# Optimization experiments

Measured on AMD Instinct MI355X. Metric: run time of the kernel, lower is better.

Reference implementation:

```python
import jax, jax.numpy as jnp
import numpy as np

B, IN, U = 16, 1024, 1024


def _wSw(W, S):
    # W: [i,u], S: [b,i,i] -> W^T S W : [b,u,u]
    return jnp.einsum('iu,bij,jv->buv', W, S, W)


def _xSx(x, Wsig):
    # (sum_i x_i^2) * W_Sigma, broadcast over batch
    return jnp.sum(x * x, axis=1)[:, None, None] * Wsig


def _trS(S, Wsig):
    return jnp.trace(S, axis1=1, axis2=2)[:, None, None] * Wsig


def _hadamard_sigma(s1, s2, m1, m2):
    # s1*s2 + diag(m1) s2 diag(m1) + diag(m2) s1 diag(m2)
    return (s1 * s2
            + m1[:, :, None] * s2 * m1[:, None, :]
            + m2[:, :, None] * s1 * m2[:, None, :])


def _act_sigma(g, S):
    # S * outer(g, g)
    return S * (g[:, :, None] * g[:, None, :])


def setup_inputs() -> dict:
    key = jax.random.key(0)
    ks = jax.random.split(key, 16)
    f32 = jnp.float32
    init_mu, ini_sigma = 0.05, -4.6
    inp = {
        'mu_inputs': jax.random.normal(ks[0], (B, IN), f32),
        'sigma_inputs': 0.01 * jax.random.normal(ks[1], (B, IN, IN), f32),
        'prev_state': 0.1 * jax.random.normal(ks[2], (B, U), f32),
        'Sigma_state': 0.01 * jax.random.normal(ks[3], (B, U, U), f32),
        'U_z': init_mu * jax.random.normal(ks[4], (IN, U), f32),
        'uz_sigma': jnp.full((U,), ini_sigma, f32),
        'W_z': init_mu * jax.random.normal(ks[5], (U, U), f32),
        'wz_sigma': jnp.full((U,), ini_sigma, f32),
        'U_r': init_mu * jax.random.normal(ks[6], (IN, U), f32),
        'ur_sigma': jnp.full((U,), ini_sigma, f32),
        'W_r': init_mu * jax.random.normal(ks[7], (U, U), f32),
        'wr_sigma': jnp.full((U,), ini_sigma, f32),
        'U_h': init_mu * jax.random.normal(ks[8], (IN, U), f32),
        'uh_sigma': jnp.full((U,), ini_sigma, f32),
        'W_h': init_mu * jax.random.normal(ks[9], (U, U), f32),
        'wh_sigma': jnp.full((U,), ini_sigma, f32),
    }
    return inp


def reference(mu_inputs, sigma_inputs, prev_state, Sigma_state,
              U_z, uz_sigma, W_z, wz_sigma,
              U_r, ur_sigma, W_r, wr_sigma,
              U_h, uh_sigma, W_h, wh_sigma):
    sp = jax.nn.softplus
    # ---- z gate ----
    pre_z = mu_inputs @ U_z + prev_state @ W_z
    z = jax.nn.sigmoid(pre_z)
    Uz_S, Wz_S = jnp.diag(sp(uz_sigma)), jnp.diag(sp(wz_sigma))
    Sigma_zz = (_wSw(U_z, sigma_inputs) + _xSx(mu_inputs, Uz_S) + _trS(sigma_inputs, Uz_S)
                + _wSw(W_z, Sigma_state) + _xSx(prev_state, Wz_S) + _trS(Sigma_state, Wz_S))
    Sigma_z = _act_sigma(z * (1.0 - z), Sigma_zz)  # analytic d sigmoid
    # ---- r gate ----
    pre_r = mu_inputs @ U_r + prev_state @ W_r
    r = jax.nn.sigmoid(pre_r)
    Ur_S, Wr_S = jnp.diag(sp(ur_sigma)), jnp.diag(sp(wr_sigma))
    Sigma_rr = (_wSw(U_r, sigma_inputs) + _xSx(mu_inputs, Ur_S) + _trS(sigma_inputs, Ur_S)
                + _wSw(W_r, Sigma_state) + _xSx(prev_state, Wr_S) + _trS(Sigma_state, Wr_S))
    Sigma_r = _act_sigma(r * (1.0 - r), Sigma_rr)
    # ---- h gate ----
    sr = prev_state * r
    pre_h = mu_inputs @ U_h + sr @ W_h
    h = jnp.tanh(pre_h)
    Uh_S, Wh_S = jnp.diag(sp(uh_sigma)), jnp.diag(sp(wh_sigma))
    sigma_g = _hadamard_sigma(Sigma_state, Sigma_r, prev_state, r)
    Sigma_hh = (_wSw(U_h, sigma_inputs) + _xSx(mu_inputs, Uh_S) + _trS(sigma_inputs, Uh_S)
                + _wSw(W_h, sigma_g) + _xSx(sr, Wh_S) + _trS(sigma_g, Wh_S))
    Sigma_h = _act_sigma(1.0 - h * h, Sigma_hh)  # analytic d tanh
    # ---- combine ----
    mu_out = z * prev_state + (1.0 - z) * h
    sigma_a = _hadamard_sigma(Sigma_z, Sigma_state, z, prev_state)
    sigma_b = _hadamard_sigma(Sigma_z, Sigma_h, 1.0 - z, h)
    sigma_ab = Sigma_z * (prev_state[:, :, None] * h[:, None, :])
    sigma_abT = Sigma_z * (h[:, :, None] * prev_state[:, None, :])
    Sigma_out = sigma_a + sigma_b - sigma_ab - sigma_abT
    Sigma_out = jnp.where(jnp.isfinite(Sigma_out), Sigma_out, jnp.zeros_like(Sigma_out))
    eye = jnp.eye(Sigma_out.shape[-1], dtype=bool)
    Sigma_out = jnp.where(eye, jnp.abs(Sigma_out), Sigma_out)
    return mu_out, Sigma_out
```

## Files before the change

kernel.cpp:

```cpp
#include <hip/hip_runtime.h>
#include <math.h>


#define B_  16
#define N_  1024
#define NN_ (1024*1024)

typedef __bf16 bf16x8 __attribute__((ext_vector_type(8)));
typedef float  f32x4  __attribute__((ext_vector_type(4)));
typedef unsigned short ushort8v __attribute__((ext_vector_type(8)));

__device__ __forceinline__ unsigned short f2bf(float f) {
  union { float f; unsigned int u; } v; v.f = f;
  unsigned int r = v.u + 0x7fffu + ((v.u >> 16) & 1u);
  return (unsigned short)(r >> 16);
}
__device__ __forceinline__ float bf2f(unsigned short h) {
  union { unsigned int u; float f; } v; v.u = ((unsigned int)h) << 16;
  return v.f;
}
__device__ __forceinline__ float f4get(const float4& v, int q) {
  return q == 0 ? v.x : (q == 1 ? v.y : (q == 2 ? v.z : v.w));
}
__device__ __forceinline__ unsigned short u4get(const ushort4& v, int q) {
  return q == 0 ? v.x : (q == 1 ? v.y : (q == 2 ? v.z : v.w));
}

__device__ __forceinline__ void gload_lds16(const void* g, void* l) {
  __builtin_amdgcn_global_load_lds((__attribute__((address_space(1))) void*)g,
                                   (__attribute__((address_space(3))) void*)l,
                                   16, 0, 0);
}

#define MFMA_ __builtin_amdgcn_mfma_f32_16x16x32_bf16

template<int OMODE, int PAIR>
__global__ __launch_bounds__(512)
void gemm8p(const unsigned short* __restrict__ A, int lda, long aStride, int koffA,
            const unsigned short* __restrict__ Bm, const unsigned short* __restrict__ Bm2,
            int ldb, long bStride, int K,
            void* __restrict__ Out, int ldo, long oStride, int noff,
            const float* __restrict__ act,
            const float* __restrict__ spU, const float* __restrict__ spW,
            const float* __restrict__ dU, const float* __restrict__ dW)
{
  __shared__ __align__(16) char ldsb[131072];
  const int id = blockIdx.x;
  const int xcd = id & 7, rest = id >> 3;
  const int mt = rest & 3, pp = rest >> 2;
  const int panel = xcd + (pp << 3);
  const int nt = panel & 3;
  const int b  = (panel >> 2) & 15;
  const int ps = PAIR ? (panel >> 6) : 0;
  const unsigned short* Bsel = (PAIR && ps) ? Bm2 : Bm;
  const int kofx = koffA + (ps ? 1024 : 0);
  const int nofx = noff  + (ps ? 1024 : 0);
  const int mbase = mt << 8, nbase = nt << 8;
  const int tid = threadIdx.x, lane = tid & 63, w = tid >> 6;
  const int wm = w >> 2, wn = w & 3;
  const int NT = K >> 6;

  f32x4 acc[8][4];
  const f32x4 zero4 = {0.f, 0.f, 0.f, 0.f};
#pragma unroll
  for (int i = 0; i < 8; i++)
#pragma unroll
    for (int j = 0; j < 4; j++) acc[i][j] = zero4;

  const int l3 = lane >> 3, l7 = lane & 7;
  const int posg = l7 ^ l3;
  const int gr = (l3 << 1) + (posg >> 2);
  const int gc = (posg & 3) << 3;
  const int bi0 = w << 1, bi1 = bi0 + 1;
  const int rS0 = ((bi0 >> 1) << 4) + gr, cS0 = ((bi0 & 1) << 5) + gc;
  const int rS1 = ((bi1 >> 1) << 4) + gr, cS1 = ((bi1 & 1) << 5) + gc;
  const unsigned short* Ab = A + (size_t)b * aStride + (size_t)mbase * lda + kofx;
  const unsigned short* Bb = Bsel + (size_t)b * bStride + (size_t)nbase * ldb;
  const int d0 = w << 11, d1 = (w << 11) + 1024;

  auto SA = [&](int tt, int h) {
    char* dst = ldsb + ((tt & 1) << 16) + (h << 14);
    const unsigned short* s = Ab + (size_t)(h << 7) * lda + ((size_t)tt << 6);
    gload_lds16(s + (size_t)rS0 * lda + cS0, dst + d0);
    gload_lds16(s + (size_t)rS1 * lda + cS1, dst + d1);
  };
  auto SB = [&](int tt, int h) {
    char* dst = ldsb + ((tt & 1) << 16) + 32768 + (h << 14);
    const unsigned short* s = Bb + (size_t)(h << 7) * ldb + ((size_t)tt << 6);
    gload_lds16(s + (size_t)rS0 * ldb + cS0, dst + d0);
    gload_lds16(s + (size_t)rS1 * ldb + cS1, dst + d1);
  };

  const int lrow = lane & 15, c4 = lane >> 4;
  const int aoff = ((lrow >> 1) << 7) + (((((lrow & 1) << 2) | c4) ^ (lrow >> 1)) << 4);
  const int abase = wm << 14;
  const int bbase = 32768 + ((wn >> 1) << 14);
  const int brg   = (wn & 1) << 2;
  auto LDA = [&](const char* pb, int mi, int ks) -> bf16x8 {
    return *(const bf16x8*)(pb + abase + (((mi << 1) + ks) << 10) + aoff);
  };
  auto LDB = [&](const char* pb, int ni, int ks) -> bf16x8 {
    return *(const bf16x8*)(pb + bbase + ((((brg + ni) << 1) + ks) << 10) + aoff);
  };

  SA(0, 0); SA(0, 1); SB(0, 0); SB(0, 1);
  if (NT > 1) { SB(1, 0); SA(1, 0); }
  asm volatile("s_waitcnt vmcnt(4)" ::: "memory");
  __builtin_amdgcn_sched_barrier(0);
  __builtin_amdgcn_s_barrier();
  __builtin_amdgcn_sched_barrier(0);

  bf16x8 av[4][2], bv[4][2];
  for (int kt = 0; kt < NT; ++kt) {
    const char* pb = ldsb + ((kt & 1) << 16);
#pragma unroll
    for (int mi = 0; mi < 4; mi++)
#pragma unroll
      for (int ks = 0; ks < 2; ks++) av[mi][ks] = LDA(pb, mi, ks);
#pragma unroll
    for (int ni = 0; ni < 2; ni++)
#pragma unroll
      for (int ks = 0; ks < 2; ks++) bv[ni][ks] = LDB(pb, ni, ks);
    if (kt + 1 < NT) SB(kt + 1, 1);
    __builtin_amdgcn_s_barrier();
    asm volatile("s_waitcnt lgkmcnt(0)" ::: "memory");
    __builtin_amdgcn_sched_barrier(0);
    __builtin_amdgcn_s_setprio(1);
#pragma unroll
    for (int ni = 0; ni < 2; ni++)
#pragma unroll
      for (int mi = 0; mi < 4; mi++) {
        acc[mi][ni] = MFMA_(av[mi][0], bv[ni][0], acc[mi][ni], 0, 0, 0);
        acc[mi][ni] = MFMA_(av[mi][1], bv[ni][1], acc[mi][ni], 0, 0, 0);
      }
    __builtin_amdgcn_s_setprio(0);
    __builtin_amdgcn_sched_barrier(0);
    __builtin_amdgcn_s_barrier();
#pragma unroll
    for (int ni = 2; ni < 4; ni++)
#pragma unroll
      for (int ks = 0; ks < 2; ks++) bv[ni][ks] = LDB(pb, ni, ks);
    if (kt + 1 < NT) SA(kt + 1, 1);
    __builtin_amdgcn_s_barrier();
    asm volatile("s_waitcnt lgkmcnt(0)" ::: "memory");
    __builtin_amdgcn_sched_barrier(0);
    __builtin_amdgcn_s_setprio(1);
#pragma unroll
    for (int ni = 2; ni < 4; ni++)
#pragma unroll
      for (int mi = 0; mi < 4; mi++) {
        acc[mi][ni] = MFMA_(av[mi][0], bv[ni][0], acc[mi][ni], 0, 0, 0);
        acc[mi][ni] = MFMA_(av[mi][1], bv[ni][1], acc[mi][ni], 0, 0, 0);
      }
    __builtin_amdgcn_s_setprio(0);
    __builtin_amdgcn_sched_barrier(0);
    __builtin_amdgcn_s_barrier();
#pragma unroll
    for (int mi = 0; mi < 4; mi++)
#pragma unroll
      for (int ks = 0; ks < 2; ks++) av[mi][ks] = LDA(pb, 4 + mi, ks);
    if (kt + 2 < NT) SB(kt + 2, 0);
    __builtin_amdgcn_s_barrier();
    asm volatile("s_waitcnt lgkmcnt(0)" ::: "memory");
    __builtin_amdgcn_sched_barrier(0);
    __builtin_amdgcn_s_setprio(1);
#pragma unroll
    for (int ni = 0; ni < 2; ni++)
#pragma unroll
      for (int mi = 0; mi < 4; mi++) {
        acc[4 + mi][ni] = MFMA_(av[mi][0], bv[ni][0], acc[4 + mi][ni], 0, 0, 0);
        acc[4 + mi][ni] = MFMA_(av[mi][1], bv[ni][1], acc[4 + mi][ni], 0, 0, 0);
      }
    __builtin_amdgcn_s_setprio(0);
    __builtin_amdgcn_sched_barrier(0);
    __builtin_amdgcn_s_barrier();
    if (kt + 2 < NT) {
      SA(kt + 2, 0);
      asm volatile("s_waitcnt vmcnt(4)" ::: "memory");
    } else {
      asm volatile("s_waitcnt vmcnt(0)" ::: "memory");
    }
    __builtin_amdgcn_sched_barrier(0);
    __builtin_amdgcn_s_barrier();
    __builtin_amdgcn_sched_barrier(0);
    __builtin_amdgcn_s_setprio(1);
#pragma unroll
    for (int ni = 2; ni < 4; ni++)
#pragma unroll
      for (int mi = 0; mi < 4; mi++) {
        acc[4 + mi][ni] = MFMA_(av[mi][0], bv[ni][0], acc[4 + mi][ni], 0, 0, 0);
        acc[4 + mi][ni] = MFMA_(av[mi][1], bv[ni][1], acc[4 + mi][ni], 0, 0, 0);
      }
    __builtin_amdgcn_s_setprio(0);
    __builtin_amdgcn_sched_barrier(0);
    __builtin_amdgcn_s_barrier();
  }

  if (OMODE == 2) {
    const float* actb = act + b * N_;
    const float dUb = dU[b], dWb = dW[b];
#pragma unroll
    for (int mi = 0; mi < 8; mi++) {
      const int u0 = mbase + wm * 128 + mi * 16 + ((lane >> 4) << 2);
#pragma unroll
      for (int ni = 0; ni < 4; ni++) {
        const int v = nbase + wn * 64 + ni * 16 + (lane & 15);
        const float avv = actb[v];
#pragma unroll
        for (int r = 0; r < 4; r++) {
          const int u = u0 + r;
          float val = acc[mi][ni][r];
          if (u == v) val += dUb * spU[u] + dWb * spW[u];
          val *= actb[u] * avv;
          ((float*)Out)[(size_t)b * oStride + (size_t)u * ldo + v] = val;
        }
      }
    }
  } else {
    __syncthreads();
    unsigned short* scr = (unsigned short*)(ldsb + w * 16384);
    const float* actb = (OMODE == 1) ? (act + b * N_) : nullptr;
    float dUb = 0.f, dWb = 0.f;
    if (OMODE == 1) { dUb = dU[b]; dWb = dW[b]; }
#pragma unroll
    for (int mi = 0; mi < 8; mi++) {
      const int rl0 = mi * 16 + ((lane >> 4) << 2);
#pragma unroll
      for (int ni = 0; ni < 4; ni++) {
        const int cl = ni * 16 + (lane & 15);
#pragma unroll
        for (int r = 0; r < 4; r++) {
          const int rl = rl0 + r;
          float val = acc[mi][ni][r];
          if (OMODE == 1) {
            const int u = mbase + wm * 128 + rl, v = nbase + wn * 64 + cl;
            if (u == v) val += dUb * spU[u] + dWb * spW[u];
            val *= actb[u] * actb[v];
          }
          scr[rl * 64 + ((((cl >> 3) ^ (rl & 7))) << 3) + (cl & 7)] = f2bf(val);
        }
      }
    }
    asm volatile("s_waitcnt lgkmcnt(0)" ::: "memory");
    __builtin_amdgcn_sched_barrier(0);
    unsigned short* ob = (unsigned short*)Out + (size_t)b * oStride
        + (size_t)(mbase + wm * 128) * ldo + nofx + nbase + wn * 64;
#pragma unroll
    for (int pq = 0; pq < 16; pq++) {
      const int row = pq * 8 + (lane >> 3);
      const int ch = (lane & 7) ^ (row & 7);
      ushort8v vv = *(const ushort8v*)&scr[row * 64 + ((lane & 7) << 3)];
      *(ushort8v*)(ob + (size_t)row * ldo + ch * 8) = vv;
    }
  }
}


__global__ void conv_bf16(const float* __restrict__ in, unsigned short* __restrict__ out, int n4)
{
  int i = blockIdx.x * 256 + threadIdx.x;
  const int stride = gridDim.x * 256;
  for (; i < n4; i += stride) {
    const float4 v = ((const float4*)in)[i];
    ushort4 o;
    o.x = f2bf(v.x); o.y = f2bf(v.y); o.z = f2bf(v.z); o.w = f2bf(v.w);
    ((ushort4*)out)[i] = o;
  }
}

__global__ void build_AT(const float* __restrict__ Uz, const float* __restrict__ Wz,
                         const float* __restrict__ Ur, const float* __restrict__ Wr,
                         const float* __restrict__ Uh, const float* __restrict__ Wh,
                         unsigned short* __restrict__ AT)
{
  __shared__ float tile[32][33];
  const int g = blockIdx.z;
  const float* U = g == 0 ? Uz : (g == 1 ? Ur : Uh);
  const float* W = g == 0 ? Wz : (g == 1 ? Wr : Wh);
  const int u0  = blockIdx.x * 32;
  const int k0g = blockIdx.y * 32;
  const float* src = (k0g >= 1024) ? W : U;
  const int kloc = k0g & 1023;
  const int tx = threadIdx.x & 31, ty = threadIdx.x >> 5;
  unsigned short* out = AT + (size_t)g * N_ * 2048;
#pragma unroll
  for (int i = 0; i < 32; i += 8) tile[ty + i][tx] = src[(size_t)(kloc + ty + i) * N_ + u0 + tx];
  __syncthreads();
#pragma unroll
  for (int i = 0; i < 32; i += 8)
    out[(size_t)(u0 + ty + i) * 2048 + k0g + tx] = f2bf(tile[tx][ty + i]);
}

__global__ void softplus6(const float* a0, const float* a1, const float* a2,
                          const float* a3, const float* a4, const float* a5,
                          float* __restrict__ sp)
{
  const float* src[6] = {a0, a1, a2, a3, a4, a5};
  const int g = blockIdx.x;
  const float* s = src[g];
  for (int i = threadIdx.x; i < N_; i += 256) {
    float x = s[i];
    sp[g * N_ + i] = (x > 20.f) ? x : log1pf(expf(x));
  }
}

__global__ void scalars1(const float* __restrict__ mu, const float* __restrict__ prev,
                         const float* __restrict__ sin_, const float* __restrict__ Sst,
                         float* __restrict__ dA, float* __restrict__ dBzr)
{
  __shared__ float red[256];
  const int b = blockIdx.x;
  float s1 = 0.f, s2 = 0.f;
  for (int i = threadIdx.x; i < N_; i += 256) {
    const float m = mu[b * N_ + i];
    s1 += m * m + sin_[(size_t)b * NN_ + (size_t)i * (N_ + 1)];
    const float p = prev[b * N_ + i];
    s2 += p * p + Sst[(size_t)b * NN_ + (size_t)i * (N_ + 1)];
  }
  red[threadIdx.x] = s1; __syncthreads();
  for (int s = 128; s > 0; s >>= 1) { if (threadIdx.x < s) red[threadIdx.x] += red[threadIdx.x + s]; __syncthreads(); }
  if (threadIdx.x == 0) dA[b] = red[0];
  __syncthreads();
  red[threadIdx.x] = s2; __syncthreads();
  for (int s = 128; s > 0; s >>= 1) { if (threadIdx.x < s) red[threadIdx.x] += red[threadIdx.x + s]; __syncthreads(); }
  if (threadIdx.x == 0) dBzr[b] = red[0];
}

__global__ __launch_bounds__(256)
void gate_pre2(const float* __restrict__ x1, const float* __restrict__ x2,
               const float* __restrict__ U0, const float* __restrict__ W0,
               const float* __restrict__ U1, const float* __restrict__ W1,
               float* __restrict__ Ppart)
{
  const int g  = blockIdx.z;
  const int ks = blockIdx.y;
  const int out = blockIdx.x * 256 + threadIdx.x;
  const int b = out >> 10, col = out & 1023;
  const float* x = (ks < 4) ? x1 : x2;
  const float* Wm = (g == 0) ? ((ks < 4) ? U0 : W0) : ((ks < 4) ? U1 : W1);
  const int k0 = (ks & 3) * 256;
  const float* xb = x + b * N_ + k0;
  const float* wp = Wm + (size_t)k0 * N_ + col;
  float acc = 0.f;
#pragma unroll 8
  for (int k = 0; k < 256; k++)
    acc += xb[k] * wp[(size_t)k * N_];
  Ppart[(g * 8 + ks) * (B_ * N_) + out] = acc;
}

__global__ void gate_act2(const float* __restrict__ P,
                          float* __restrict__ z, float* __restrict__ gz,
                          float* __restrict__ r, float* __restrict__ gr)
{
  const int out = blockIdx.x * 256 + threadIdx.x;
  float a0 = 0.f, a1 = 0.f;
#pragma unroll
  for (int ks = 0; ks < 8; ks++) {
    a0 += P[ks * (B_ * N_) + out];
    a1 += P[(8 + ks) * (B_ * N_) + out];
  }
  const float s0 = 1.f / (1.f + expf(-a0));
  const float s1 = 1.f / (1.f + expf(-a1));
  z[out] = s0; gz[out] = s0 * (1.f - s0);
  r[out] = s1; gr[out] = s1 * (1.f - s1);
}

__global__ __launch_bounds__(256)
void gate_pre1(const float* __restrict__ x1, const float* __restrict__ x2,
               const float* __restrict__ U0, const float* __restrict__ W0,
               float* __restrict__ Ppart)
{
  const int ks = blockIdx.y;
  const int out = blockIdx.x * 256 + threadIdx.x;
  const int b = out >> 10, col = out & 1023;
  const float* x = (ks < 4) ? x1 : x2;
  const float* Wm = (ks < 4) ? U0 : W0;
  const int k0 = (ks & 3) * 256;
  const float* xb = x + b * N_ + k0;
  const float* wp = Wm + (size_t)k0 * N_ + col;
  float acc = 0.f;
#pragma unroll 8
  for (int k = 0; k < 256; k++)
    acc += xb[k] * wp[(size_t)k * N_];
  Ppart[ks * (B_ * N_) + out] = acc;
}

__global__ void gate_act1(const float* __restrict__ P,
                          float* __restrict__ h, float* __restrict__ gh)
{
  const int out = blockIdx.x * 256 + threadIdx.x;
  float a0 = 0.f;
#pragma unroll
  for (int ks = 0; ks < 8; ks++) a0 += P[ks * (B_ * N_) + out];
  const float s = tanhf(a0);
  h[out] = s; gh[out] = 1.f - s * s;
}

__global__ void sr_csr(const float* __restrict__ prev, const float* __restrict__ r,
                       float* __restrict__ sr, float* __restrict__ csr)
{
  __shared__ float red[256];
  const int b = blockIdx.x;
  float s = 0.f;
  for (int i = threadIdx.x; i < N_; i += 256) {
    const float v = prev[b * N_ + i] * r[b * N_ + i];
    sr[b * N_ + i] = v;
    s += v * v;
  }
  red[threadIdx.x] = s; __syncthreads();
  for (int k = 128; k > 0; k >>= 1) { if (threadIdx.x < k) red[threadIdx.x] += red[threadIdx.x + k]; __syncthreads(); }
  if (threadIdx.x == 0) csr[b] = red[0];
}

__global__ void hadamard_sg(const float* __restrict__ Sst, unsigned short* __restrict__ Sg,
                            const float* __restrict__ prev, const float* __restrict__ r)
{
  const size_t idx = ((size_t)blockIdx.x * 256 + threadIdx.x) * 4;
  const int b = (int)(idx >> 20);
  const int rem = (int)(idx & (NN_ - 1));
  const int i = rem >> 10, j0 = rem & 1023;
  const float pi = prev[b * N_ + i], ri = r[b * N_ + i];
  const float4  ss  = *(const float4*)(Sst + (size_t)b * NN_ + rem);
  const ushort4 sr4 = *(const ushort4*)(Sg + (size_t)b * NN_ + rem);
  ushort4 o;
  unsigned short* op = (unsigned short*)&o;
#pragma unroll
  for (int q = 0; q < 4; q++) {
    const float srv = bf2f(u4get(sr4, q));
    const float stv = f4get(ss, q);
    const float pj = prev[b * N_ + j0 + q];
    const float rj = r[b * N_ + j0 + q];
    op[q] = f2bf(stv * srv + pi * pj * srv + ri * rj * stv);
  }
  *(ushort4*)(Sg + (size_t)b * NN_ + rem) = o;
}

__global__ void scalars2(const unsigned short* __restrict__ Sg,
                         const float* __restrict__ csr, float* __restrict__ dBh)
{
  __shared__ float red[256];
  const int b = blockIdx.x;
  float s = 0.f;
  for (int i = threadIdx.x; i < N_; i += 256)
    s += bf2f(Sg[(size_t)b * NN_ + (size_t)i * (N_ + 1)]);
  red[threadIdx.x] = s; __syncthreads();
  for (int k = 128; k > 0; k >>= 1) { if (threadIdx.x < k) red[threadIdx.x] += red[threadIdx.x + k]; __syncthreads(); }
  if (threadIdx.x == 0) dBh[b] = red[0] + csr[b];
}

__global__ void mu_kernel(const float* __restrict__ z, const float* __restrict__ prev,
                          const float* __restrict__ h, float* __restrict__ mu_out)
{
  const int i = blockIdx.x * 256 + threadIdx.x;
  const float zz = z[i];
  mu_out[i] = zz * prev[i] + (1.f - zz) * h[i];
}

__global__ void combine(const unsigned short* __restrict__ Sz, const float* __restrict__ Sst,
                        const float* __restrict__ z, const float* __restrict__ prev,
                        const float* __restrict__ h, float* __restrict__ SigOut)
{
  const int row = blockIdx.x;
  const int b = row >> 10, u = row & 1023;
  const float zu = z[b * N_ + u], pu = prev[b * N_ + u], hu = h[b * N_ + u];
  const size_t base = (size_t)b * NN_ + (size_t)u * N_;
  const int j0 = threadIdx.x * 4;
  const ushort4 s4 = *(const ushort4*)(Sz + base + j0);
  const float4 sh = *(const float4*)(SigOut + base + j0);
  const float4 st = *(const float4*)(Sst + base + j0);
  const float4 zv = *(const float4*)(z + b * N_ + j0);
  const float4 pv = *(const float4*)(prev + b * N_ + j0);
  const float4 hv = *(const float4*)(h + b * N_ + j0);
  float o[4];
#pragma unroll
  for (int q = 0; q < 4; q++) {
    const int v = j0 + q;
    const float sz  = bf2f(u4get(s4, q));
    const float shh = f4get(sh, q);
    const float stt = f4get(st, q);
    const float zvv = f4get(zv, q);
    const float pvv = f4get(pv, q);
    const float hvv = f4get(hv, q);
    float res = sz * stt + zu * zvv * stt + pu * pvv * sz
              + sz * shh + (1.f - zu) * (1.f - zvv) * shh + hu * hvv * sz
              - sz * (pu * hvv) - sz * (hu * pvv);
    if (!isfinite(res)) res = 0.f;
    if (u == v) res = fabsf(res);
    o[q] = res;
  }
  float4 ov; ov.x = o[0]; ov.y = o[1]; ov.z = o[2]; ov.w = o[3];
  *(float4*)(SigOut + base + j0) = ov;
}


extern "C" void kernel_launch(void* const* d_in, const int* in_sizes, int n_in,
                              void* d_out, int out_size, void* d_ws, size_t ws_size,
                              hipStream_t stream)
{
  const float* mu   = (const float*)d_in[0];
  const float* sin_ = (const float*)d_in[1];
  const float* prev = (const float*)d_in[2];
  const float* Sst  = (const float*)d_in[3];
  const float* Uz = (const float*)d_in[4];  const float* uzs = (const float*)d_in[5];
  const float* Wz = (const float*)d_in[6];  const float* wzs = (const float*)d_in[7];
  const float* Ur = (const float*)d_in[8];  const float* urs = (const float*)d_in[9];
  const float* Wr = (const float*)d_in[10]; const float* wrs = (const float*)d_in[11];
  const float* Uh = (const float*)d_in[12]; const float* uhs = (const float*)d_in[13];
  const float* Wh = (const float*)d_in[14]; const float* whs = (const float*)d_in[15];

  char* ws = (char*)d_ws;
  size_t off = 0;
  auto take = [&](size_t bytes) -> char* {
    char* p = ws + off;
    off = (off + bytes + 255) & ~(size_t)255;
    return p;
  };
  unsigned short* Tcm = (unsigned short*)take((size_t)B_ * 2048 * 1024 * 2);
  unsigned short* Sz  = (unsigned short*)take((size_t)B_ * NN_ * 2);
  unsigned short* Sg  = (unsigned short*)take((size_t)B_ * NN_ * 2);
  unsigned short* AT  = (unsigned short*)take((size_t)3 * N_ * 2048 * 2);
  float* Ppart = (float*)take((size_t)16 * B_ * N_ * 4);
  float* sp   = (float*)take(6 * N_ * 4);
  float* z    = (float*)take(B_ * N_ * 4);
  float* gz   = (float*)take(B_ * N_ * 4);
  float* rr   = (float*)take(B_ * N_ * 4);
  float* gr   = (float*)take(B_ * N_ * 4);
  float* h    = (float*)take(B_ * N_ * 4);
  float* gh   = (float*)take(B_ * N_ * 4);
  float* sr   = (float*)take(B_ * N_ * 4);
  float* dA   = (float*)take(64);
  float* dBzr = (float*)take(64);
  float* dBh  = (float*)take(64);
  float* csr  = (float*)take(64);
  if (off > ws_size) return;

  float* mu_out = (float*)d_out;
  float* SigOut = (float*)d_out + (size_t)B_ * N_;
  unsigned short* SinH = (unsigned short*)SigOut;
  unsigned short* SstH = (unsigned short*)SigOut + (size_t)B_ * NN_;

  const unsigned short* ATz = AT;
  const unsigned short* ATr = AT + (size_t)N_ * 2048;
  const unsigned short* ATh = AT + (size_t)2 * N_ * 2048;

  conv_bf16<<<2048, 256, 0, stream>>>(sin_, SinH, B_ * NN_ / 4);
  conv_bf16<<<2048, 256, 0, stream>>>(Sst,  SstH, B_ * NN_ / 4);
  softplus6<<<6, 256, 0, stream>>>(uzs, wzs, urs, wrs, uhs, whs, sp);
  scalars1<<<16, 256, 0, stream>>>(mu, prev, sin_, Sst, dA, dBzr);
  build_AT<<<dim3(32, 64, 3), 256, 0, stream>>>(Uz, Wz, Ur, Wr, Uh, Wh, AT);
  gate_pre2<<<dim3(64, 8, 2), 256, 0, stream>>>(mu, prev, Uz, Wz, Ur, Wr, Ppart);
  gate_act2<<<64, 256, 0, stream>>>(Ppart, z, gz, rr, gr);
  sr_csr<<<16, 256, 0, stream>>>(prev, rr, sr, csr);
  gate_pre1<<<dim3(64, 8), 256, 0, stream>>>(mu, sr, Uh, Wh, Ppart);
  gate_act1<<<64, 256, 0, stream>>>(Ppart, h, gh);

  const long tS = (long)2048 * 1024;

  gemm8p<0, 1><<<512, 512, 0, stream>>>(ATz, 2048, 0, 0, SinH, SstH, 1024, (long)NN_, 1024,
                                        Tcm, 2048, tS, 0, nullptr, nullptr, nullptr, nullptr, nullptr);
  gemm8p<1, 0><<<256, 512, 0, stream>>>(ATz, 2048, 0, 0, Tcm, nullptr, 2048, tS, 2048,
                                        Sz, 1024, (long)NN_, 0, gz, sp + 0, sp + 1024, dA, dBzr);
  gemm8p<0, 1><<<512, 512, 0, stream>>>(ATr, 2048, 0, 0, SinH, SstH, 1024, (long)NN_, 1024,
                                        Tcm, 2048, tS, 0, nullptr, nullptr, nullptr, nullptr, nullptr);
  gemm8p<1, 0><<<256, 512, 0, stream>>>(ATr, 2048, 0, 0, Tcm, nullptr, 2048, tS, 2048,
                                        Sg, 1024, (long)NN_, 0, gr, sp + 2048, sp + 3072, dA, dBzr);
  hadamard_sg<<<16384, 256, 0, stream>>>(Sst, Sg, prev, rr);
  scalars2<<<16, 256, 0, stream>>>(Sg, csr, dBh);
  gemm8p<0, 1><<<512, 512, 0, stream>>>(ATh, 2048, 0, 0, SinH, Sg, 1024, (long)NN_, 1024,
                                        Tcm, 2048, tS, 0, nullptr, nullptr, nullptr, nullptr, nullptr);
  gemm8p<2, 0><<<256, 512, 0, stream>>>(ATh, 2048, 0, 0, Tcm, nullptr, 2048, tS, 2048,
                                        SigOut, 1024, (long)NN_, 0, gh, sp + 4096, sp + 5120, dA, dBh);
  mu_kernel<<<64, 256, 0, stream>>>(z, prev, h, mu_out);
  combine<<<16384, 256, 0, stream>>>(Sz, Sst, z, prev, h, SigOut);
}
```

Measured before the change: 568.3 us.

## Restructure GEMM main loop to split phases by k-substep instead of n-half

Reorganizes the 4-phase GEMM inner loop so each phase loads a single k-substep (ks) of A/B fragments and issues 16 MFMAs over all 4 n-columns, rather than splitting by n-halves with both ks. The global-to-LDS prefetch schedule is reordered to match: A for the next tile is staged in the early phases, and both B halves for tile kt+2 in the last phase. The goal is to cut live fragment registers (av/bv halved) and rebalance LDS reads against MFMAs, at the cost of reloading B fragments twice per tile and changing when the LDS buffers are overwritten, which risks races if the reorder is wrong.

```diff
diff --git a/kernel.cpp b/kernel.cpp
--- a/kernel.cpp
+++ b/kernel.cpp
@@ -104,93 +104,80 @@
   };
 
   SA(0, 0); SA(0, 1); SB(0, 0); SB(0, 1);
-  if (NT > 1) { SB(1, 0); SA(1, 0); }
+  if (NT > 1) { SB(1, 0); SB(1, 1); }
   asm volatile("s_waitcnt vmcnt(4)" ::: "memory");
   __builtin_amdgcn_sched_barrier(0);
   __builtin_amdgcn_s_barrier();
   __builtin_amdgcn_sched_barrier(0);
 
-  bf16x8 av[4][2], bv[4][2];
+  bf16x8 av[4], bv[4];
   for (int kt = 0; kt < NT; ++kt) {
     const char* pb = ldsb + ((kt & 1) << 16);
 #pragma unroll
-    for (int mi = 0; mi < 4; mi++)
-#pragma unroll
-      for (int ks = 0; ks < 2; ks++) av[mi][ks] = LDA(pb, mi, ks);
-#pragma unroll
-    for (int ni = 0; ni < 2; ni++)
-#pragma unroll
-      for (int ks = 0; ks < 2; ks++) bv[ni][ks] = LDB(pb, ni, ks);
-    if (kt + 1 < NT) SB(kt + 1, 1);
+    for (int mi = 0; mi < 4; mi++) av[mi] = LDA(pb, mi, 0);
+#pragma unroll
+    for (int ni = 0; ni < 4; ni++) bv[ni] = LDB(pb, ni, 0);
+    if (kt + 1 < NT) SA(kt + 1, 0);
     __builtin_amdgcn_s_barrier();
     asm volatile("s_waitcnt lgkmcnt(0)" ::: "memory");
     __builtin_amdgcn_sched_barrier(0);
     __builtin_amdgcn_s_setprio(1);
 #pragma unroll
-    for (int ni = 0; ni < 2; ni++)
-#pragma unroll
-      for (int mi = 0; mi < 4; mi++) {
-        acc[mi][ni] = MFMA_(av[mi][0], bv[ni][0], acc[mi][ni], 0, 0, 0);
-        acc[mi][ni] = MFMA_(av[mi][1], bv[ni][1], acc[mi][ni], 0, 0, 0);
-      }
+    for (int ni = 0; ni < 4; ni++)
+#pragma unroll
+      for (int mi = 0; mi < 4; mi++)
+        acc[mi][ni] = MFMA_(av[mi], bv[ni], acc[mi][ni], 0, 0, 0);
     __builtin_amdgcn_s_setprio(0);
     __builtin_amdgcn_sched_barrier(0);
     __builtin_amdgcn_s_barrier();
 #pragma unroll
-    for (int ni = 2; ni < 4; ni++)
-#pragma unroll
-      for (int ks = 0; ks < 2; ks++) bv[ni][ks] = LDB(pb, ni, ks);
+    for (int mi = 0; mi < 4; mi++) av[mi] = LDA(pb, 4 + mi, 0);
     if (kt + 1 < NT) SA(kt + 1, 1);
     __builtin_amdgcn_s_barrier();
     asm volatile("s_waitcnt lgkmcnt(0)" ::: "memory");
     __builtin_amdgcn_sched_barrier(0);
     __builtin_amdgcn_s_setprio(1);
 #pragma unroll
-    for (int ni = 2; ni < 4; ni++)
-#pragma unroll
-      for (int mi = 0; mi < 4; mi++) {
-        acc[mi][ni] = MFMA_(av[mi][0], bv[ni][0], acc[mi][ni], 0, 0, 0);
-        acc[mi][ni] = MFMA_(av[mi][1], bv[ni][1], acc[mi][ni], 0, 0, 0);
-      }
+    for (int ni = 0; ni < 4; ni++)
+#pragma unroll
+      for (int mi = 0; mi < 4; mi++)
+        acc[4 + mi][ni] = MFMA_(av[mi], bv[ni], acc[4 + mi][ni], 0, 0, 0);
     __builtin_amdgcn_s_setprio(0);
     __builtin_amdgcn_sched_barrier(0);
     __builtin_amdgcn_s_barrier();
 #pragma unroll
-    for (int mi = 0; mi < 4; mi++)
-#pragma unroll
-      for (int ks = 0; ks < 2; ks++) av[mi][ks] = LDA(pb, 4 + mi, ks);
-    if (kt + 2 < NT) SB(kt + 2, 0);
+    for (int mi = 0; mi < 4; mi++) av[mi] = LDA(pb, mi, 1);
+#pragma unroll
+    for (int ni = 0; ni < 4; ni++) bv[ni] = LDB(pb, ni, 1);
     __builtin_amdgcn_s_barrier();
     asm volatile("s_waitcnt lgkmcnt(0)" ::: "memory");
     __builtin_amdgcn_sched_barrier(0);
     __builtin_amdgcn_s_setprio(1);
 #pragma unroll
-    for (int ni = 0; ni < 2; ni++)
-#pragma unroll
-      for (int mi = 0; mi < 4; mi++) {
-        acc[4 + mi][ni] = MFMA_(av[mi][0], bv[ni][0], acc[4 + mi][ni], 0, 0, 0);
-        acc[4 + mi][ni] = MFMA_(av[mi][1], bv[ni][1], acc[4 + mi][ni], 0, 0, 0);
-      }
+    for (int ni = 0; ni < 4; ni++)
+#pragma unroll
+      for (int mi = 0; mi < 4; mi++)
+        acc[mi][ni] = MFMA_(av[mi], bv[ni], acc[mi][ni], 0, 0, 0);
     __builtin_amdgcn_s_setprio(0);
     __builtin_amdgcn_sched_barrier(0);
     __builtin_amdgcn_s_barrier();
+#pragma unroll
+    for (int mi = 0; mi < 4; mi++) av[mi] = LDA(pb, 4 + mi, 1);
     if (kt + 2 < NT) {
-      SA(kt + 2, 0);
+      SB(kt + 2, 0); SB(kt + 2, 1);
       asm volatile("s_waitcnt vmcnt(4)" ::: "memory");
     } else {
       asm volatile("s_waitcnt vmcnt(0)" ::: "memory");
     }
-    __builtin_amdgcn_sched_barrier(0);
-    __builtin_amdgcn_s_barrier();
+    __builtin_amdgcn_s_barrier();
+    asm volatile("s_waitcnt lgkmcnt(0)" ::: "memory");
     __builtin_amdgcn_sched_barrier(0);
     __builtin_amdgcn_s_setprio(1);
 #pragma unroll
-    for (int ni = 2; ni < 4; ni++)
-#pragma unroll
-      for (int mi = 0; mi < 4; mi++) {
-        acc[4 + mi][ni] = MFMA_(av[mi][0], bv[ni][0], acc[4 + mi][ni], 0, 0, 0);
-        acc[4 + mi][ni] = MFMA_(av[mi][1], bv[ni][1], acc[4 + mi][ni], 0, 0, 0);
-      }
+    for (int ni = 0; ni < 4; ni++)
+#pragma unroll
+      for (int mi = 0; mi < 4; mi++)
+        acc[4 + mi][ni] = MFMA_(av[mi], bv[ni], acc[4 + mi][ni], 0, 0, 0);
     __builtin_amdgcn_s_setprio(0);
     __builtin_amdgcn_sched_barrier(0);
     __builtin_amdgcn_s_barrier();
```

Result: no change. 575.1 us (+1.2%).
